# Kernel tuning notes

Measured on AMD Instinct MI355X. Metric: run time of the kernel, lower is better.

## Reference

```python
import jax, jax.numpy as jnp
import numpy as np

N = 200000   # num_nodes
D = 64       # embedding_dims
B = 4096     # batch of target nodes (batched per-edge processing)
K = 128      # padded in-neighbor count per target
W = 20       # window_size (history deque length)
H = 128      # hidden_size


def setup_inputs() -> dict:
    key = jax.random.key(0)
    ks = jax.random.split(key, 14)
    return {
        "adj_time": jax.random.uniform(ks[0], (N,), jnp.float32),          # last-seen times in [0,1)
        "gc": jax.random.uniform(ks[1], (N,), jnp.float32),                 # per-node centrality scalar (dict_gc)
        "cur_time": jnp.ones((1,), jnp.float32),                            # current event time (>= all stored times)
        "neigh_mask": jnp.ones((B, K), jnp.float32),                        # 1 = valid neighbor slot
        "hist_feat": jax.random.normal(ks[2], (B, W, 2 * D), jnp.float32),  # feature_dict[...]['feature'] deque
        "hist_time": jax.random.uniform(ks[3], (B, W), jnp.float32),        # feature_dict[...]['time'] deque
        "t2v_w": jax.random.normal(ks[4], (D,), jnp.float32),               # Time2Vec('cos') weights
        "t2v_b": jax.random.normal(ks[5], (D,), jnp.float32),
        "node_w": jax.random.normal(ks[6], (D,), jnp.float32),              # linear_node: Linear(1, D)
        "node_b": jax.random.normal(ks[7], (D,), jnp.float32),
        "att_w": jax.random.normal(ks[8], (2 * D,), jnp.float32),           # Attention: score = cat(a,b) @ w + b
        "att_b": jax.random.normal(ks[9], (1,), jnp.float32),
        "weight": jax.random.normal(ks[10], (H, 4 * D), jnp.float32) * 0.05,
        "targets": jax.random.randint(ks[11], (B,), 0, N),
        "neigh_idx": jax.random.randint(ks[12], (B, K), 0, N),
    }


def reference(adj_time, gc, cur_time, neigh_mask, hist_feat, hist_time,
              t2v_w, t2v_b, node_w, node_b, att_w, att_b, weight,
              targets, neigh_idx):
    t = cur_time[0]

    def node_encoding(idx):
        # Time2Vec('cos'): first channel linear, rest cos(w*dt+b)
        dt = jnp.abs(t - adj_time[idx])[..., None]            # [..., 1]
        phase = t2v_w * dt + t2v_b                            # [..., D]
        tv = jnp.concatenate([phase[..., :1], jnp.cos(phase[..., 1:])], axis=-1)
        feat = jax.nn.relu(tv + gc[idx][..., None] * node_w + node_b)
        # F.normalize (L2 over feature dim)
        return feat / jnp.maximum(jnp.linalg.norm(feat, axis=-1, keepdims=True), 1e-12)

    tgt_feat = node_encoding(targets)       # [B, D]
    ngh_feat = node_encoding(neigh_idx)     # [B, K, D]

    # Decayer(2, 'log'): time_score = 1 / (2 * log(e + dt))
    time_score = 1.0 / (2.0 * jnp.log(jnp.e + (t - adj_time[neigh_idx])))   # [B, K]
    # Attention score between target and each neighbor encoding
    att = (tgt_feat @ att_w[:D])[:, None] \
        + jnp.einsum("bkd,d->bk", ngh_feat, att_w[D:]) + att_b[0]           # [B, K]
    score = jax.nn.leaky_relu(time_score + att, 0.01) * neigh_mask          # [B, K]
    neigh_agg = jnp.einsum("bk,bkd->bd", score, ngh_feat)                   # [B, D]

    combined = jnp.concatenate([tgt_feat, neigh_agg], axis=-1)              # [B, 2D]

    # History aggregation with Decayer(2, 'rev'): w = 1 / (2 * (1 + dt))
    hist_w = 1.0 / (2.0 * (1.0 + (t - hist_time)))                          # [B, W]
    hist_agg = jnp.einsum("bw,bwd->bd", hist_w, hist_feat)                  # [B, 2D]

    feat4 = jnp.concatenate([hist_agg, combined], axis=-1)                  # [B, 4D]
    return jax.nn.relu(feat4 @ weight.T)                                    # [B, H]
```

## Files before the change

### kernel.cpp

```cpp
#include <hip/hip_runtime.h>
#include <math.h>

#define NN 200000
#define DD 64
#define BB 4096
#define KK 128
#define WW 20
#define HH 128
#define TPB 512
#define RPB 4

__device__ __forceinline__ float fast_rcp(float x) { return __builtin_amdgcn_rcpf(x); }
__device__ __forceinline__ float fast_rsq(float x) { return __builtin_amdgcn_rsqf(x); }
__device__ __forceinline__ float readlane_f(float v, int l) {
    return __builtin_bit_cast(float, __builtin_amdgcn_readlane(__builtin_bit_cast(int, v), l));
}

__global__ __launch_bounds__(512, 8) void fused(
    const float* __restrict__ adj_time, const float* __restrict__ gc,
    const float* __restrict__ cur_time, const float* __restrict__ neigh_mask,
    const float* __restrict__ hist_feat, const float* __restrict__ hist_time,
    const float* __restrict__ t2v_w, const float* __restrict__ t2v_b,
    const float* __restrict__ node_w, const float* __restrict__ node_b,
    const float* __restrict__ att_w, const float* __restrict__ att_b,
    const float* __restrict__ weight,
    const int* __restrict__ targets, const int* __restrict__ neigh_idx,
    float* __restrict__ out)
{
    const int b0   = blockIdx.x * RPB;
    const int tid  = threadIdx.x;
    const int lane = tid & 63;
    const int wv   = tid >> 6;
    const int r_   = tid >> 7;
    const int d_   = tid & 127;

    __shared__ float hws[RPB][WW];
    __shared__ float stL[RPB];
    __shared__ float tile[RPB * 256];
    __shared__ float aggp[8][64];
    __shared__ float wl[128 * 36];

    const float t = cur_time[0];

    float m_k, at, g, dt, ts_k;
    {
        int idx = neigh_idx[b0 * KK + tid];
        m_k     = neigh_mask[b0 * KK + tid];
        at      = adj_time[idx];
        g       = gc[idx];
        dt      = fabsf(t - at);
        ts_k    = fast_rcp(2.0f * __logf(2.71828182845904523536f + (t - at)));
    }
    if (tid < RPB * WW) {
        int r = tid / WW, w = tid - r * WW;
        hws[r][w] = fast_rcp(2.0f * (1.0f + (t - hist_time[(b0 + r) * WW + w])));
    }
    if (wv < RPB) {
        int   tg  = targets[b0 + wv];
        float dtT = fabsf(t - adj_time[tg]);
        float gT  = gc[tg];
        float ph  = fmaf(t2v_w[lane], dtT, t2v_b[lane]);
        float tv_ = (lane == 0) ? ph : __cosf(ph);
        float f   = fmaxf(tv_ + fmaf(gT, node_w[lane], node_b[lane]), 0.f);
        float ss  = f * f;
#pragma unroll
        for (int off = 32; off; off >>= 1) ss += __shfl_xor(ss, off, 64);
        float invn = fast_rsq(fmaxf(ss, 1e-24f));
        float tfn  = f * invn;
        float sdt  = tfn * att_w[lane];
#pragma unroll
        for (int off = 32; off; off >>= 1) sdt += __shfl_xor(sdt, off, 64);
        if (lane == 0) stL[wv] = sdt;
        tile[wv * 256 + 128 + lane] = tfn;
    }
    __syncthreads();

    float wk;
    {
        float s2 = 0.f, sd = 0.f;
#pragma unroll 8
        for (int d = 0; d < 64; ++d) {
            float ph  = fmaf(t2v_w[d], dt, t2v_b[d]);
            float cv  = __cosf(ph);
            float tv_ = (d == 0) ? ph : cv;
            float f   = fmaxf(tv_ + fmaf(g, node_w[d], node_b[d]), 0.f);
            s2 = fmaf(f, f, s2);
            sd = fmaf(f, att_w[64 + d], sd);
        }
        float invn = fast_rsq(fmaxf(s2, 1e-24f));
        float sc   = ts_k + stL[r_] + sd * invn + att_b[0];
        sc = (sc > 0.f) ? sc : 0.01f * sc;
        wk = sc * m_k * invn;
    }

    {
        const float* hf = hist_feat + (size_t)(b0 + r_) * WW * 128 + d_;
        float s = 0.f;
#pragma unroll
        for (int w = 0; w < WW; ++w) s = fmaf(hws[r_][w], hf[w * 128], s);
        tile[r_ * 256 + d_] = s;
    }

    {
        float pw = t2v_w[lane], pb = t2v_b[lane];
        float nw = node_w[lane], nb2 = node_b[lane];
        float acc = 0.f;
#pragma unroll
        for (int j = 0; j < 64; ++j) {
            float dtj = readlane_f(dt, j);
            float gj  = readlane_f(g,  j);
            float wkj = readlane_f(wk, j);
            float ph  = fmaf(pw, dtj, pb);
            float cv  = __cosf(ph);
            float tv_ = (lane == 0) ? ph : cv;
            float f   = fmaxf(tv_ + fmaf(gj, nw, nb2), 0.f);
            acc = fmaf(wkj, f, acc);
        }
        aggp[wv][lane] = acc;
    }
    __syncthreads();

    if (!(wv & 1))
        tile[(wv >> 1) * 256 + 192 + lane] = aggp[wv][lane] + aggp[wv | 1][lane];
    __syncthreads();

    const int h = tid & 127;
    float4 t4 = *(const float4*)(tile + r_ * 256 + 4 * lane);
    float acc = 0.f;

    for (int c = 0; c < 8; ++c) {
        __syncthreads();
#pragma unroll
        for (int i = 0; i < 2; ++i) {
            int l  = i * TPB + tid;
            int hh = l >> 3;
            int q8 = (l & 7) * 4;
            float4 w4 = *(const float4*)(weight + hh * 256 + c * 32 + q8);
            *(float4*)(wl + hh * 36 + q8) = w4;
        }
        __syncthreads();

#pragma unroll
        for (int q = 0; q < 8; ++q) {
            float4 w4 = *(const float4*)(wl + h * 36 + 4 * q);
            int src = c * 8 + q;
            float tx = readlane_f(t4.x, src);
            float ty = readlane_f(t4.y, src);
            float tz = readlane_f(t4.z, src);
            float tw = readlane_f(t4.w, src);
            acc += w4.x * tx + w4.y * ty + w4.z * tz + w4.w * tw;
        }
    }

    out[(size_t)(b0 + r_) * 128 + h] = fmaxf(acc, 0.f);
}

extern "C" void kernel_launch(void* const* d_in, const int* in_sizes, int n_in,
                              void* d_out, int out_size, void* d_ws, size_t ws_size,
                              hipStream_t stream) {
    const float* adj_time  = (const float*)d_in[0];
    const float* gc        = (const float*)d_in[1];
    const float* cur_time  = (const float*)d_in[2];
    const float* neigh_mask= (const float*)d_in[3];
    const float* hist_feat = (const float*)d_in[4];
    const float* hist_time = (const float*)d_in[5];
    const float* t2v_w     = (const float*)d_in[6];
    const float* t2v_b     = (const float*)d_in[7];
    const float* node_w    = (const float*)d_in[8];
    const float* node_b    = (const float*)d_in[9];
    const float* att_w     = (const float*)d_in[10];
    const float* att_b     = (const float*)d_in[11];
    const float* weight    = (const float*)d_in[12];
    const int*   targets   = (const int*)d_in[13];
    const int*   neigh_idx = (const int*)d_in[14];

    float* out = (float*)d_out;

    fused<<<BB / RPB, TPB, 0, stream>>>(adj_time, gc, cur_time, neigh_mask,
                                        hist_feat, hist_time, t2v_w, t2v_b,
                                        node_w, node_b, att_w, att_b, weight,
                                        targets, neigh_idx, out);
}
```

Baseline: 137.9 us.

## Read weight rows directly from global in final GEMV, drop LDS weight staging

The final projection no longer stages weight chunks through LDS across 8 synchronized passes. Each thread now reads its weight row straight from global or L2 as float4, and the feature row from a padded LDS tile, with four lanes sharing one hidden unit across the four batch rows. This removes 16 barriers and the LDS copy, at the cost of more global or L2 weight traffic per block and uncoalesced row-strided reads. The per-neighbor loop is also peeled so d=0 no longer needs a per-iteration select, and the tile stride is padded to reduce bank conflicts.

```diff
diff --git a/kernel.cpp b/kernel.cpp
--- a/kernel.cpp
+++ b/kernel.cpp
@@ -9,6 +9,7 @@
 #define HH 128
 #define TPB 512
 #define RPB 4
+#define TSTRIDE 260
 
 __device__ __forceinline__ float fast_rcp(float x) { return __builtin_amdgcn_rcpf(x); }
 __device__ __forceinline__ float fast_rsq(float x) { return __builtin_amdgcn_rsqf(x); }
@@ -36,20 +37,19 @@
 
     __shared__ float hws[RPB][WW];
     __shared__ float stL[RPB];
-    __shared__ float tile[RPB * 256];
+    __shared__ float tile[RPB * TSTRIDE];
     __shared__ float aggp[8][64];
-    __shared__ float wl[128 * 36];
 
     const float t = cur_time[0];
 
-    float m_k, at, g, dt, ts_k;
+    float m_k, g, dt, ts_k;
     {
         int idx = neigh_idx[b0 * KK + tid];
         m_k     = neigh_mask[b0 * KK + tid];
-        at      = adj_time[idx];
+        float a = adj_time[idx];
         g       = gc[idx];
-        dt      = fabsf(t - at);
-        ts_k    = fast_rcp(2.0f * __logf(2.71828182845904523536f + (t - at)));
+        dt      = fabsf(t - a);
+        ts_k    = fast_rcp(2.0f * __logf(2.71828182845904523536f + (t - a)));
     }
     if (tid < RPB * WW) {
         int r = tid / WW, w = tid - r * WW;
@@ -71,19 +71,20 @@
 #pragma unroll
         for (int off = 32; off; off >>= 1) sdt += __shfl_xor(sdt, off, 64);
         if (lane == 0) stL[wv] = sdt;
-        tile[wv * 256 + 128 + lane] = tfn;
+        tile[wv * TSTRIDE + 128 + lane] = tfn;
     }
     __syncthreads();
 
     float wk;
     {
-        float s2 = 0.f, sd = 0.f;
-#pragma unroll 8
-        for (int d = 0; d < 64; ++d) {
-            float ph  = fmaf(t2v_w[d], dt, t2v_b[d]);
-            float cv  = __cosf(ph);
-            float tv_ = (d == 0) ? ph : cv;
-            float f   = fmaxf(tv_ + fmaf(g, node_w[d], node_b[d]), 0.f);
+        float ph0 = fmaf(t2v_w[0], dt, t2v_b[0]);
+        float f0  = fmaxf(ph0 + fmaf(g, node_w[0], node_b[0]), 0.f);
+        float s2  = f0 * f0;
+        float sd  = f0 * att_w[64];
+#pragma unroll 9
+        for (int d = 1; d < 64; ++d) {
+            float ph = fmaf(t2v_w[d], dt, t2v_b[d]);
+            float f  = fmaxf(__cosf(ph) + fmaf(g, node_w[d], node_b[d]), 0.f);
             s2 = fmaf(f, f, s2);
             sd = fmaf(f, att_w[64 + d], sd);
         }
@@ -98,7 +99,7 @@
         float s = 0.f;
 #pragma unroll
         for (int w = 0; w < WW; ++w) s = fmaf(hws[r_][w], hf[w * 128], s);
-        tile[r_ * 256 + d_] = s;
+        tile[r_ * TSTRIDE + d_] = s;
     }
 
     {
@@ -121,38 +122,23 @@
     __syncthreads();
 
     if (!(wv & 1))
-        tile[(wv >> 1) * 256 + 192 + lane] = aggp[wv][lane] + aggp[wv | 1][lane];
+        tile[(wv >> 1) * TSTRIDE + 192 + lane] = aggp[wv][lane] + aggp[wv | 1][lane];
     __syncthreads();
 
-    const int h = tid & 127;
-    float4 t4 = *(const float4*)(tile + r_ * 256 + 4 * lane);
-    float acc = 0.f;
-
-    for (int c = 0; c < 8; ++c) {
-        __syncthreads();
-#pragma unroll
-        for (int i = 0; i < 2; ++i) {
-            int l  = i * TPB + tid;
-            int hh = l >> 3;
-            int q8 = (l & 7) * 4;
-            float4 w4 = *(const float4*)(weight + hh * 256 + c * 32 + q8);
-            *(float4*)(wl + hh * 36 + q8) = w4;
+    {
+        const int h = wv * 16 + (lane >> 2);
+        const int r = lane & 3;
+        const float4* wrow = (const float4*)(weight + (size_t)h * 256);
+        const float*  tb   = tile + r * TSTRIDE;
+        float acc = 0.f;
+#pragma unroll 8
+        for (int j = 0; j < 64; ++j) {
+            float4 w4 = wrow[j];
+            float4 f4 = *(const float4*)(tb + 4 * j);
+            acc += w4.x * f4.x + w4.y * f4.y + w4.z * f4.z + w4.w * f4.w;
         }
-        __syncthreads();
-
-#pragma unroll
-        for (int q = 0; q < 8; ++q) {
-            float4 w4 = *(const float4*)(wl + h * 36 + 4 * q);
-            int src = c * 8 + q;
-            float tx = readlane_f(t4.x, src);
-            float ty = readlane_f(t4.y, src);
-            float tz = readlane_f(t4.z, src);
-            float tw = readlane_f(t4.w, src);
-            acc += w4.x * tx + w4.y * ty + w4.z * tz + w4.w * tw;
-        }
+        out[(size_t)(b0 + r) * 128 + h] = fmaxf(acc, 0.f);
     }
-
-    out[(size_t)(b0 + r_) * 128 + h] = fmaxf(acc, 0.f);
 }
 
 extern "C" void kernel_launch(void* const* d_in, const int* in_sizes, int n_in,
```

Result: no change. 137.5 us (-0.3%).
